# Optimization experiments

Measured on AMD Instinct MI355X. Metric: run time of the kernel, lower is better.

Reference implementation:

```python
import jax, jax.numpy as jnp
import numpy as np

BITS = 4
GROUPSIZE = 128
IN_FEATURES = 4096
OUT_FEATURES = 4096
GROUPS = IN_FEATURES // GROUPSIZE  # 32
TOKENS = 8192


def setup_inputs() -> dict:
    key = jax.random.key(0)
    k_x, k_s, k_b = jax.random.split(key, 3)
    rng = np.random.default_rng(0)
    # packed 4-bit weights: 8 nibbles per int32 word
    qweight = jnp.asarray(
        rng.integers(-2**31, 2**31, size=(IN_FEATURES // 8, OUT_FEATURES), dtype=np.int64).astype(np.int32)
    )
    qzeros = jnp.asarray(
        rng.integers(-2**31, 2**31, size=(GROUPS, OUT_FEATURES // 8), dtype=np.int64).astype(np.int32)
    )
    scales = jax.random.uniform(k_s, (GROUPS, OUT_FEATURES), dtype=jnp.float32) * 0.02 + 0.001
    g_idx = (jnp.arange(IN_FEATURES, dtype=jnp.int32) // GROUPSIZE).astype(jnp.int32)
    bias = jax.random.normal(k_b, (OUT_FEATURES,), dtype=jnp.float32) * 0.01
    x = jax.random.normal(k_x, (TOKENS, IN_FEATURES), dtype=jnp.float32)
    return {"x": x, "qweight": qweight, "qzeros": qzeros, "scales": scales,
            "g_idx": g_idx, "bias": bias}


def reference(x, qweight, qzeros, scales, g_idx, bias):
    out_features = qweight.shape[1]
    in_features = qweight.shape[0] * 8
    mask = jnp.int32(15)  # 2**bits - 1
    wf = jnp.arange(0, 32, BITS, dtype=jnp.int32)  # [8] nibble shift amounts
    # unpack zero points: [groups, out//8, 8] -> [groups, out]
    zeros = ((qzeros[:, :, None] >> wf[None, None, :]) & mask) + 1
    zeros = zeros.reshape(scales.shape)
    # unpack weights: [in//8, 8, out] -> [in, out]
    weight = (qweight[:, None, :] >> wf[None, :, None]) & mask
    weight = weight.reshape(in_features, out_features)
    # dequantize per group and matmul
    W = scales[g_idx] * (weight - zeros[g_idx]).astype(scales.dtype)
    out = x @ W
    return out + bias
```

## Files before the change

kernel.cpp:

```cpp
#include <hip/hip_runtime.h>
#include <cstdint>
#include <cstddef>

#define IN_F   4096
#define OUT_F  4096
#define NTOK   8192
#define NGRP   32

#define BM 256
#define BN 256
#define BK 64
#define KTILES   (IN_F / BK)
#define LDS_TILE (BM * BK)

typedef __attribute__((ext_vector_type(8))) __bf16 bf16x8;
typedef __attribute__((ext_vector_type(4))) float  floatx4;

__device__ __forceinline__ unsigned short f2bf(float f) {
    unsigned int u = __builtin_bit_cast(unsigned int, f);
    u += 0x7fffu + ((u >> 16) & 1u);
    return (unsigned short)(u >> 16);
}

__device__ __forceinline__ void gload16(const void* g, void* l) {
    __builtin_amdgcn_global_load_lds(
        (const __attribute__((address_space(1))) void*)g,
        (__attribute__((address_space(3))) void*)l,
        16, 0, 0);
}

__global__ void dequant_kernel(const int* __restrict__ qweight,
                               const int* __restrict__ qzeros,
                               const float* __restrict__ scales,
                               const int* __restrict__ g_idx,
                               unsigned short* __restrict__ Wt) {
    __shared__ unsigned short tile[256 * 64];
    const int tk  = blockIdx.x & 63;
    const int tn  = blockIdx.x >> 6;
    const int tid = threadIdx.x;
    const int n   = tn * 256 + tid;

#pragma unroll
    for (int r = 0; r < 8; ++r) {
        const int k8 = tk * 8 + r;
        const int k  = k8 * 8;
        const int g  = g_idx[k];
        const int qw = qweight[(size_t)k8 * OUT_F + n];
        const float s = scales[g * OUT_F + n];
        const int  zw = qzeros[g * (OUT_F / 8) + (n >> 3)];
        const float z = (float)(((zw >> (4 * (n & 7))) & 15) + 1);
        const float sz = s * z;
        union { unsigned short h[8]; uint4 v; } u;
#pragma unroll
        for (int j = 0; j < 8; ++j)
            u.h[j] = f2bf(s * (float)((qw >> (4 * j)) & 15) - sz);
        *(uint4*)(tile + tid * 64 + ((r ^ (tid & 7)) * 8)) = u.v;
    }
    __syncthreads();
#pragma unroll
    for (int i = 0; i < 8; ++i) {
        const int nl = i * 32 + (tid >> 3);
        const int c  = tid & 7;
        const uint4 v = *(const uint4*)(tile + nl * 64 + ((c ^ (nl & 7)) * 8));
        *(uint4*)(Wt + (size_t)(tn * 256 + nl) * IN_F + tk * 64 + c * 8) = v;
    }
}

__global__ void xcast_kernel(const float* __restrict__ x,
                             unsigned short* __restrict__ Xb) {
    const size_t i = ((size_t)blockIdx.x * 256 + threadIdx.x) * 8;
    const float4 a = *(const float4*)(x + i);
    const float4 b = *(const float4*)(x + i + 4);
    union { unsigned short h[8]; uint4 v; } u;
    u.h[0] = f2bf(a.x); u.h[1] = f2bf(a.y); u.h[2] = f2bf(a.z); u.h[3] = f2bf(a.w);
    u.h[4] = f2bf(b.x); u.h[5] = f2bf(b.y); u.h[6] = f2bf(b.z); u.h[7] = f2bf(b.w);
    *(uint4*)(Xb + i) = u.v;
}

#define VMCNT4() asm volatile("s_waitcnt vmcnt(4)" ::: "memory")
#define VMCNT2() asm volatile("s_waitcnt vmcnt(2)" ::: "memory")
#define VMCNT0() asm volatile("s_waitcnt vmcnt(0)" ::: "memory")
#define BARRIER() do { __builtin_amdgcn_s_barrier(); asm volatile("" ::: "memory"); } while (0)

template<int I0, int J0>
__device__ __forceinline__ void quad(floatx4 (&acc)[8][4],
                                     const bf16x8 (&av)[4][2],
                                     const bf16x8 (&bv)[4][2]) {
#pragma unroll
    for (int i4 = 0; i4 < 4; ++i4)
#pragma unroll
        for (int jj = 0; jj < 2; ++jj)
#pragma unroll
            for (int kk = 0; kk < 2; ++kk)
                acc[I0 + i4][J0 + jj] = __builtin_amdgcn_mfma_f32_16x16x32_bf16(
                    av[i4][kk], bv[J0 + jj][kk], acc[I0 + i4][J0 + jj], 0, 0, 0);
}

__global__ __launch_bounds__(512, 2) void gemm_kernel(
        const unsigned short* __restrict__ Xb,
        const unsigned short* __restrict__ Wt,
        const float* __restrict__ bias,
        float* __restrict__ out) {
    __shared__ unsigned short As[2 * LDS_TILE];
    __shared__ unsigned short Bs[2 * LDS_TILE];

    const int tid  = threadIdx.x;
    const int wave = tid >> 6;
    const int lane = tid & 63;
    const int mi   = lane & 15;
    const int kq   = lane >> 4;

    const int bid = blockIdx.x;
    const int swz = (bid & 7) * 64 + (bid >> 3);
    const int m0  = (swz >> 4) * BM;
    const int n0  = (swz & 15) * BN;

    const int wrow = (wave >> 2) * 128;
    const int wcol = (wave & 3) * 64;

    const int lrow   = lane >> 3;
    const int lchunk = ((lane & 7) ^ lrow) * 8;
    const unsigned short* aSrc = Xb + (size_t)(m0 + lrow) * IN_F + lchunk;
    const unsigned short* bSrc = Wt + (size_t)(n0 + lrow) * IN_F + lchunk;

    const int raA = (wave >> 2) * 128 + (wave & 3) * 16;
    const int raB = (wave >> 1) * 64  + (wave & 1) * 16;

    const int aRd = (wrow + mi) * BK;
    const int bRd = (wcol + mi) * BK;
    const int cp0 = ((kq)     ^ (mi & 7)) * 8;
    const int cp1 = ((4 + kq) ^ (mi & 7)) * 8;

    floatx4 acc[8][4];
#pragma unroll
    for (int i = 0; i < 8; ++i)
#pragma unroll
        for (int j = 0; j < 4; ++j)
            acc[i][j] = floatx4{0.f, 0.f, 0.f, 0.f};

    bf16x8 av[4][2], bv[4][2];

    auto stageA = [&](int bufofs, int h, int kt) {
        const int r0 = raA + h * 64;
        gload16(aSrc + (size_t)(r0 + 0) * IN_F + (size_t)kt * BK,
                (void*)(As + bufofs + (r0 + 0) * BK));
        gload16(aSrc + (size_t)(r0 + 8) * IN_F + (size_t)kt * BK,
                (void*)(As + bufofs + (r0 + 8) * BK));
    };
    auto stageB = [&](int bufofs, int h, int kt) {
        const int r0 = raB + h * 32;
        gload16(bSrc + (size_t)(r0 + 0) * IN_F + (size_t)kt * BK,
                (void*)(Bs + bufofs + (r0 + 0) * BK));
        gload16(bSrc + (size_t)(r0 + 8) * IN_F + (size_t)kt * BK,
                (void*)(Bs + bufofs + (r0 + 8) * BK));
    };
    auto ldah = [&](int bufofs, int ah) {
#pragma unroll
        for (int i4 = 0; i4 < 4; ++i4) {
            av[i4][0] = *(const bf16x8*)(As + bufofs + aRd + (ah * 4 + i4) * (16 * BK) + cp0);
            av[i4][1] = *(const bf16x8*)(As + bufofs + aRd + (ah * 4 + i4) * (16 * BK) + cp1);
        }
    };
    auto ldb01 = [&](int bufofs) {
#pragma unroll
        for (int jj = 0; jj < 2; ++jj) {
            bv[jj][0] = *(const bf16x8*)(Bs + bufofs + bRd + jj * (16 * BK) + cp0);
            bv[jj][1] = *(const bf16x8*)(Bs + bufofs + bRd + jj * (16 * BK) + cp1);
        }
    };
    auto ldb23 = [&](int bufofs) {
#pragma unroll
        for (int jj = 0; jj < 2; ++jj) {
            bv[2 + jj][0] = *(const bf16x8*)(Bs + bufofs + bRd + (2 + jj) * (16 * BK) + cp0);
            bv[2 + jj][1] = *(const bf16x8*)(Bs + bufofs + bRd + (2 + jj) * (16 * BK) + cp1);
        }
    };

    stageA(0, 0, 0);
    stageB(0, 0, 0);
    stageB(0, 1, 0);
    stageA(0, 1, 0);
    VMCNT4();
    BARRIER();

    for (int kt = 0; kt < KTILES - 1; ++kt) {
        const int bo = (kt & 1) * LDS_TILE;
        const int no = bo ^ LDS_TILE;
        const int kn = kt + 1;

        ldah(bo, 0); ldb01(bo);
        stageA(no, 0, kn);
        VMCNT4();
        BARRIER();
        __builtin_amdgcn_s_setprio(1);
        quad<0, 0>(acc, av, bv);
        __builtin_amdgcn_s_setprio(0);
        BARRIER();

        ldb23(bo);
        stageB(no, 0, kn);
        VMCNT4();
        BARRIER();
        __builtin_amdgcn_s_setprio(1);
        quad<0, 2>(acc, av, bv);
        __builtin_amdgcn_s_setprio(0);
        BARRIER();

        ldah(bo, 1);
        stageB(no, 1, kn);
        BARRIER();
        __builtin_amdgcn_s_setprio(1);
        quad<4, 2>(acc, av, bv);
        __builtin_amdgcn_s_setprio(0);
        BARRIER();

        stageA(no, 1, kn);
        VMCNT4();
        BARRIER();
        __builtin_amdgcn_s_setprio(1);
        quad<4, 0>(acc, av, bv);
        __builtin_amdgcn_s_setprio(0);
        BARRIER();
    }

    {
        const int bo = ((KTILES - 1) & 1) * LDS_TILE;
        ldah(bo, 0); ldb01(bo);
        VMCNT2();
        BARRIER();
        __builtin_amdgcn_s_setprio(1);
        quad<0, 0>(acc, av, bv);
        __builtin_amdgcn_s_setprio(0);
        BARRIER();

        ldb23(bo);
        VMCNT0();
        BARRIER();
        __builtin_amdgcn_s_setprio(1);
        quad<0, 2>(acc, av, bv);
        __builtin_amdgcn_s_setprio(0);
        BARRIER();

        ldah(bo, 1);
        __builtin_amdgcn_s_setprio(1);
        quad<4, 2>(acc, av, bv);
        quad<4, 0>(acc, av, bv);
        __builtin_amdgcn_s_setprio(0);
    }

    const int mq = kq;
#pragma unroll
    for (int j = 0; j < 4; ++j) {
        const int col = n0 + wcol + j * 16 + mi;
        const float bb = bias[col];
#pragma unroll
        for (int i = 0; i < 8; ++i) {
#pragma unroll
            for (int r = 0; r < 4; ++r) {
                const int row = m0 + wrow + i * 16 + mq * 4 + r;
                out[(size_t)row * OUT_F + col] = acc[i][j][r] + bb;
            }
        }
    }
}

extern "C" void kernel_launch(void* const* d_in, const int* in_sizes, int n_in,
                              void* d_out, int out_size, void* d_ws, size_t ws_size,
                              hipStream_t stream) {
    const float* x       = (const float*)d_in[0];
    const int*   qweight = (const int*)d_in[1];
    const int*   qzeros  = (const int*)d_in[2];
    const float* scales  = (const float*)d_in[3];
    const int*   g_idx   = (const int*)d_in[4];
    const float* bias    = (const float*)d_in[5];
    float*       out     = (float*)d_out;

    unsigned short* Wt = (unsigned short*)d_ws;
    unsigned short* Xb = Wt + (size_t)OUT_F * IN_F;

    dequant_kernel<<<64 * 16, 256, 0, stream>>>(qweight, qzeros, scales, g_idx, Wt);
    xcast_kernel<<<((size_t)NTOK * IN_F / 8) / 256, 256, 0, stream>>>(x, Xb);

    gemm_kernel<<<dim3((NTOK / BM) * (OUT_F / BN)), 512, 0, stream>>>(Xb, Wt, bias, out);
}
```

Before: 507.7 us.

## Prefetch half-tiles two steps ahead and add explicit LDS waits with sched barriers

Restructures the GEMM main loop so the first halves of the next-next K tile are staged into the just-consumed buffer, giving global loads a deeper lead over the MFMA work. Adds explicit lgkmcnt waits and sched_barrier fences so LDS reads complete before each MFMA quad and the compiler cannot reorder across phases. The loop now peels two epilogue iterations. This changes buffer-reuse timing and risks races if the barrier placement is wrong.

```diff
diff --git a/kernel.cpp b/kernel.cpp
--- a/kernel.cpp
+++ b/kernel.cpp
@@ -77,10 +77,14 @@
     *(uint4*)(Xb + i) = u.v;
 }
 
-#define VMCNT4() asm volatile("s_waitcnt vmcnt(4)" ::: "memory")
-#define VMCNT2() asm volatile("s_waitcnt vmcnt(2)" ::: "memory")
-#define VMCNT0() asm volatile("s_waitcnt vmcnt(0)" ::: "memory")
-#define BARRIER() do { __builtin_amdgcn_s_barrier(); asm volatile("" ::: "memory"); } while (0)
+#define VMCNT4()   asm volatile("s_waitcnt vmcnt(4)" ::: "memory")
+#define VMCNT0()   asm volatile("s_waitcnt vmcnt(0)" ::: "memory")
+#define LGKMCNT0() asm volatile("s_waitcnt lgkmcnt(0)" ::: "memory")
+#define LGKMCNT8() asm volatile("s_waitcnt lgkmcnt(8)" ::: "memory")
+#define SCHEDB()   __builtin_amdgcn_sched_barrier(0)
+#define BAR() do { asm volatile("" ::: "memory"); \
+                   __builtin_amdgcn_s_barrier();  \
+                   asm volatile("" ::: "memory"); } while (0)
 
 template<int I0, int J0>
 __device__ __forceinline__ void quad(floatx4 (&acc)[8][4],
@@ -180,68 +184,105 @@
     stageB(0, 0, 0);
     stageB(0, 1, 0);
     stageA(0, 1, 0);
+    stageA(LDS_TILE, 0, 1);
+    stageB(LDS_TILE, 0, 1);
     VMCNT4();
-    BARRIER();
-
-    for (int kt = 0; kt < KTILES - 1; ++kt) {
+    BAR();
+
+    for (int kt = 0; kt < KTILES - 2; ++kt) {
         const int bo = (kt & 1) * LDS_TILE;
         const int no = bo ^ LDS_TILE;
-        const int kn = kt + 1;
 
         ldah(bo, 0); ldb01(bo);
-        stageA(no, 0, kn);
+        stageB(no, 1, kt + 1);
+        LGKMCNT8();
+        BAR();
+        LGKMCNT0(); SCHEDB();
+        __builtin_amdgcn_s_setprio(1);
+        quad<0, 0>(acc, av, bv);
+        __builtin_amdgcn_s_setprio(0);
+        BAR();
+
+        ldb23(bo);
+        stageA(no, 1, kt + 1);
+        BAR();
+        LGKMCNT0(); SCHEDB();
+        __builtin_amdgcn_s_setprio(1);
+        quad<0, 2>(acc, av, bv);
+        __builtin_amdgcn_s_setprio(0);
+        BAR();
+
+        ldah(bo, 1);
+        BAR();
+        LGKMCNT0(); SCHEDB();
+        __builtin_amdgcn_s_setprio(1);
+        quad<4, 2>(acc, av, bv);
+        __builtin_amdgcn_s_setprio(0);
+        BAR();
+
+        stageA(bo, 0, kt + 2);
+        stageB(bo, 0, kt + 2);
         VMCNT4();
-        BARRIER();
+        BAR();
+        SCHEDB();
+        __builtin_amdgcn_s_setprio(1);
+        quad<4, 0>(acc, av, bv);
+        __builtin_amdgcn_s_setprio(0);
+        BAR();
+    }
+
+    {
+        const int bo = 0, no = LDS_TILE;
+        ldah(bo, 0); ldb01(bo);
+        stageB(no, 1, 63);
+        LGKMCNT8();
+        BAR();
+        LGKMCNT0(); SCHEDB();
         __builtin_amdgcn_s_setprio(1);
         quad<0, 0>(acc, av, bv);
         __builtin_amdgcn_s_setprio(0);
-        BARRIER();
+        BAR();
 
         ldb23(bo);
-        stageB(no, 0, kn);
-        VMCNT4();
-        BARRIER();
+        stageA(no, 1, 63);
+        BAR();
+        LGKMCNT0(); SCHEDB();
         __builtin_amdgcn_s_setprio(1);
         quad<0, 2>(acc, av, bv);
         __builtin_amdgcn_s_setprio(0);
-        BARRIER();
+        BAR();
 
         ldah(bo, 1);
-        stageB(no, 1, kn);
-        BARRIER();
+        BAR();
+        LGKMCNT0(); SCHEDB();
         __builtin_amdgcn_s_setprio(1);
         quad<4, 2>(acc, av, bv);
         __builtin_amdgcn_s_setprio(0);
-        BARRIER();
-
-        stageA(no, 1, kn);
-        VMCNT4();
-        BARRIER();
+        BAR();
+
+        VMCNT0();
+        BAR();
+        SCHEDB();
         __builtin_amdgcn_s_setprio(1);
         quad<4, 0>(acc, av, bv);
         __builtin_amdgcn_s_setprio(0);
-        BARRIER();
+        BAR();
     }
 
     {
-        const int bo = ((KTILES - 1) & 1) * LDS_TILE;
+        const int bo = LDS_TILE;
         ldah(bo, 0); ldb01(bo);
-        VMCNT2();
-        BARRIER();
+        LGKMCNT0(); SCHEDB();
         __builtin_amdgcn_s_setprio(1);
         quad<0, 0>(acc, av, bv);
         __builtin_amdgcn_s_setprio(0);
-        BARRIER();
-
         ldb23(bo);
-        VMCNT0();
-        BARRIER();
+        LGKMCNT0(); SCHEDB();
         __builtin_amdgcn_s_setprio(1);
         quad<0, 2>(acc, av, bv);
         __builtin_amdgcn_s_setprio(0);
-        BARRIER();
-
         ldah(bo, 1);
+        LGKMCNT0(); SCHEDB();
         __builtin_amdgcn_s_setprio(1);
         quad<4, 2>(acc, av, bv);
         quad<4, 0>(acc, av, bv);
```

Measured after the change: 528.2 us. +4.0%, slower.
